# Kernel optimization log

Measured on AMD Instinct MI355X. Metric: run time of the kernel, lower is better.

The kernel has to match this reference:

```python
import jax, jax.numpy as jnp
import numpy as np

EPS = 1e-8

def setup_inputs() -> dict:
    key = jax.random.key(0)
    k1, k2, k3, k4, k5 = jax.random.split(key, 5)
    B, C_in, C_out, H, W, S, K = 16, 128, 128, 128, 128, 512, 3
    return {
        "x": jax.random.normal(k1, (B, C_in, H, W), dtype=jnp.float32),
        "style": jax.random.normal(k2, (B, S), dtype=jnp.float32),
        "weight": jax.random.normal(k3, (1, C_out, C_in, K, K), dtype=jnp.float32),
        "mod_w": jax.random.normal(k4, (C_in, S), dtype=jnp.float32) * 0.05,
        "mod_b": jax.random.normal(k5, (C_in,), dtype=jnp.float32) * 0.05,
    }

def _modulated_weights(style, weight, mod_w, mod_b):
    # style: [B, S] -> s: [B, C_in]
    s = style @ mod_w.T + mod_b
    # w: [B, C_out, C_in, K, K]
    w = weight * s[:, None, :, None, None]
    # demodulation: rsqrt of sum of squares over (C_in, K, K)
    decoef = jax.lax.rsqrt(jnp.sum(w * w, axis=(2, 3, 4)) + EPS)  # [B, C_out]
    return w * decoef[:, :, None, None, None]

def _conv_one(xi, wi):
    # xi: [C_in, H, W], wi: [C_out, C_in, K, K]; 'SAME' padding (K//2)
    out = jax.lax.conv_general_dilated(
        xi[None], wi,
        window_strides=(1, 1), padding="SAME",
        dimension_numbers=("NCHW", "OIHW", "NCHW"))
    return out[0]

def reference(x, style, weight, mod_w, mod_b):
    w = _modulated_weights(style, weight, mod_w, mod_b)  # [B, C_out, C_in, K, K]
    # per-sample conv (equivalent to groups=B grouped conv in torch)
    return jax.vmap(_conv_one)(x, w)  # [B, C_out, H, W]
```

## Files before the change

kernel.cpp:

```cpp
#include <hip/hip_runtime.h>
#include <hip/hip_bf16.h>


#define Bn 16
#define Cc 128
#define HW 128
#define Sv 512

typedef __bf16 bf16x8 __attribute__((ext_vector_type(8)));
typedef float f32x4 __attribute__((ext_vector_type(4)));
typedef unsigned short ushort8 __attribute__((ext_vector_type(8)));

static __device__ __forceinline__ unsigned short bf16bits(float f) {
    return __builtin_bit_cast(unsigned short, __float2bfloat16(f));
}

static __device__ __forceinline__ void gl_lds16(const void* g, void* l) {
    __builtin_amdgcn_global_load_lds(
        (const __attribute__((address_space(1))) unsigned int*)g,
        (__attribute__((address_space(3))) unsigned int*)l, 16, 0, 0);
}

__global__ __launch_bounds__(64) void k_style(const float* __restrict__ style,
                                              const float* __restrict__ mod_w,
                                              const float* __restrict__ mod_b,
                                              float* __restrict__ s_out) {
    int b = blockIdx.x >> 7, ci = blockIdx.x & 127;
    int lane = threadIdx.x;
    const float* st = style + (size_t)b * Sv;
    const float* mw = mod_w + (size_t)ci * Sv;
    float acc = 0.f;
#pragma unroll
    for (int k = 0; k < Sv; k += 64)
        acc += st[k + lane] * mw[k + lane];
#pragma unroll
    for (int off = 32; off > 0; off >>= 1)
        acc += __shfl_down(acc, off, 64);
    if (lane == 0) s_out[b * Cc + ci] = acc + mod_b[ci];
}

__global__ __launch_bounds__(128) void k_mod(const float* __restrict__ weight,
                                             const float* __restrict__ s,
                                             __hip_bfloat16* __restrict__ wsW) {
    int b = blockIdx.x >> 7;
    int co = blockIdx.x & 127;
    int ci = threadIdx.x;
    float sv = s[b * Cc + ci];
    const float* wp = weight + ((size_t)co * Cc + ci) * 9;
    float wv[9];
    float ss = 0.f;
#pragma unroll
    for (int j = 0; j < 9; j++) {
        wv[j] = wp[j] * sv;
        ss += wv[j] * wv[j];
    }
    __shared__ float red[128];
    red[ci] = ss;
    __syncthreads();
    for (int s2 = 64; s2 > 0; s2 >>= 1) {
        if (ci < s2) red[ci] += red[ci + s2];
        __syncthreads();
    }
    float dec = rsqrtf(red[0] + 1e-8f);
    int pos = ((((ci >> 3) ^ (co & 7)) << 3) | (ci & 7));
#pragma unroll
    for (int j = 0; j < 9; j++) {
        wsW[(((size_t)b * 9 + j) * Cc + co) * Cc + pos] = __float2bfloat16(wv[j] * dec);
    }
}

__global__ __launch_bounds__(256, 2) void k_conv(const float* __restrict__ x,
                                                 const __hip_bfloat16* __restrict__ wsW,
                                                 float* __restrict__ out) {
    __shared__ __align__(16) __bf16 Xs[130 * 128];
    __shared__ __align__(16) __bf16 Ws[128 * 128];

    int bx = blockIdx.x;
    int b = bx >> 7, h = bx & 127;
    int t = threadIdx.x;
    int lane = t & 63;
    int wvid = t >> 6;
    int wave_m = wvid >> 1, wave_n = wvid & 1;
    int l15 = lane & 15, quad = lane >> 4;

    f32x4 acc[4][4] = {};

    const float* xb = x + (size_t)b * (Cc * HW * HW);
    const __hip_bfloat16* wbase = wsW + (size_t)b * 9 * (Cc * Cc);

    if (t < 32) {
        int row = (t < 16) ? 0 : 129;
        int g = t & 15;
        *(bf16x8*)(&Xs[row * 128 + g * 8]) = (bf16x8){};
    }

    for (int kh = 0; kh < 3; kh++) {
        int hp = h + kh - 1;
        if ((unsigned)hp >= (unsigned)HW) continue;

        __syncthreads();
        const float* xr = xb + (size_t)hp * HW;
#pragma unroll
        for (int it = 0; it < 8; it++) {
            int id = it * 256 + t;
            int w = id & 127;
            int cig = id >> 7;
            const float* p = xr + (size_t)cig * 8 * (HW * HW) + w;
            ushort8 pk;
#pragma unroll
            for (int j = 0; j < 8; j++)
                pk[j] = bf16bits(p[(size_t)j * (HW * HW)]);
            int row = w + 1;
            int g2 = cig ^ (row & 7);
            *(bf16x8*)(&Xs[row * 128 + (g2 << 3)]) = __builtin_bit_cast(bf16x8, pk);
        }

        for (int kw = 0; kw < 3; kw++) {
            __syncthreads();
            const __hip_bfloat16* wsrc = wbase + (size_t)(kh * 3 + kw) * (Cc * Cc);
#pragma unroll
            for (int it = 0; it < 8; it++) {
                int chunk = wvid * 8 + it;
                gl_lds16(wsrc + chunk * 512 + lane * 8, &Ws[chunk * 512]);
            }
            __syncthreads();
#pragma unroll
            for (int ks = 0; ks < 4; ks++) {
                int kg = ks * 4 + quad;
                bf16x8 a[4], bfr[4];
#pragma unroll
                for (int mi = 0; mi < 4; mi++) {
                    int co = wave_m * 64 + mi * 16 + l15;
                    a[mi] = *(const bf16x8*)(&Ws[co * 128 + ((kg ^ (co & 7)) << 3)]);
                }
#pragma unroll
                for (int ni = 0; ni < 4; ni++) {
                    int row = wave_n * 64 + ni * 16 + l15 + kw;
                    bfr[ni] = *(const bf16x8*)(&Xs[row * 128 + ((kg ^ (row & 7)) << 3)]);
                }
#pragma unroll
                for (int mi = 0; mi < 4; mi++)
#pragma unroll
                    for (int ni = 0; ni < 4; ni++)
                        acc[mi][ni] = __builtin_amdgcn_mfma_f32_16x16x32_bf16(a[mi], bfr[ni], acc[mi][ni], 0, 0, 0);
            }
        }
    }

    float* ob = out + (size_t)b * (Cc * HW * HW) + h * HW;
#pragma unroll
    for (int mi = 0; mi < 4; mi++) {
#pragma unroll
        for (int ni = 0; ni < 4; ni++) {
            int w = wave_n * 64 + ni * 16 + l15;
#pragma unroll
            for (int r = 0; r < 4; r++) {
                int co = wave_m * 64 + mi * 16 + quad * 4 + r;
                ob[(size_t)co * (HW * HW) + w] = acc[mi][ni][r];
            }
        }
    }
}

extern "C" void kernel_launch(void* const* d_in, const int* in_sizes, int n_in,
                              void* d_out, int out_size, void* d_ws, size_t ws_size,
                              hipStream_t stream) {
    const float* x      = (const float*)d_in[0];
    const float* style  = (const float*)d_in[1];
    const float* weight = (const float*)d_in[2];
    const float* mod_w  = (const float*)d_in[3];
    const float* mod_b  = (const float*)d_in[4];
    float* out = (float*)d_out;

    float* s_ws = (float*)d_ws;
    __hip_bfloat16* wsW = (__hip_bfloat16*)((char*)d_ws + 8192);

    k_style<<<Bn * Cc, 64, 0, stream>>>(style, mod_w, mod_b, s_ws);
    k_mod<<<Bn * Cc, 128, 0, stream>>>(weight, s_ws, wsW);
    k_conv<<<Bn * HW, 256, 0, stream>>>(x, wsW, out);
}
```

Before: 299.5 us.

## Compute two output rows per block, sharing weights and four preloaded input rows

Each conv block now covers two output rows with 512 threads. It preloads four bf16 input rows into LDS once and shares each staged 3x3 weight slice across both rows. Horizontal padding moves from extra LDS rows to clamped indices with zeroing, and block indices are remapped so neighbouring blocks share a batch. This halves weight traffic per output row and drops the per-kh input reload and barriers. In exchange LDS grows to about 160KB, which likely allows only one block per CU, and all input loads happen up front with no overlap.

```diff
diff --git a/kernel.cpp b/kernel.cpp
--- a/kernel.cpp
+++ b/kernel.cpp
@@ -69,18 +69,23 @@
     }
 }
 
-__global__ __launch_bounds__(256, 2) void k_conv(const float* __restrict__ x,
+__global__ __launch_bounds__(512, 2) void k_conv(const float* __restrict__ x,
                                                  const __hip_bfloat16* __restrict__ wsW,
                                                  float* __restrict__ out) {
-    __shared__ __align__(16) __bf16 Xs[130 * 128];
+    __shared__ __align__(16) __bf16 Xs[4 * 128 * 128];
     __shared__ __align__(16) __bf16 Ws[128 * 128];
 
-    int bx = blockIdx.x;
-    int b = bx >> 7, h = bx & 127;
+    int bx0 = blockIdx.x;
+    int bx = (bx0 & 7) * 128 + (bx0 >> 3);
+    int b = bx >> 6;
+    int h0 = (bx & 63) << 1;
+
     int t = threadIdx.x;
     int lane = t & 63;
-    int wvid = t >> 6;
-    int wave_m = wvid >> 1, wave_n = wvid & 1;
+    int wv = t >> 6;
+    int m2 = wv >> 2;
+    int th = (wv >> 1) & 1;
+    int n2 = wv & 1;
     int l15 = lane & 15, quad = lane >> 4;
 
     f32x4 acc[4][4] = {};
@@ -88,74 +93,76 @@
     const float* xb = x + (size_t)b * (Cc * HW * HW);
     const __hip_bfloat16* wbase = wsW + (size_t)b * 9 * (Cc * Cc);
 
-    if (t < 32) {
-        int row = (t < 16) ? 0 : 129;
-        int g = t & 15;
-        *(bf16x8*)(&Xs[row * 128 + g * 8]) = (bf16x8){};
+    for (int j = 0; j < 4; j++) {
+        int hp = h0 - 1 + j;
+        bool ok = (unsigned)hp < (unsigned)HW;
+        const float* xr = xb + (size_t)hp * HW;
+#pragma unroll
+        for (int c = 0; c < 4; c++) {
+            int id = c * 512 + t;
+            int w = id & 127;
+            int g = id >> 7;
+            ushort8 pk = {};
+            if (ok) {
+                const float* p = xr + (size_t)g * 8 * (HW * HW) + w;
+#pragma unroll
+                for (int e = 0; e < 8; e++)
+                    pk[e] = bf16bits(p[(size_t)e * (HW * HW)]);
+            }
+            *(bf16x8*)(&Xs[j * 16384 + w * 128 + ((g ^ (w & 7)) << 3)]) =
+                __builtin_bit_cast(bf16x8, pk);
+        }
     }
 
     for (int kh = 0; kh < 3; kh++) {
-        int hp = h + kh - 1;
-        if ((unsigned)hp >= (unsigned)HW) continue;
-
-        __syncthreads();
-        const float* xr = xb + (size_t)hp * HW;
-#pragma unroll
-        for (int it = 0; it < 8; it++) {
-            int id = it * 256 + t;
-            int w = id & 127;
-            int cig = id >> 7;
-            const float* p = xr + (size_t)cig * 8 * (HW * HW) + w;
-            ushort8 pk;
-#pragma unroll
-            for (int j = 0; j < 8; j++)
-                pk[j] = bf16bits(p[(size_t)j * (HW * HW)]);
-            int row = w + 1;
-            int g2 = cig ^ (row & 7);
-            *(bf16x8*)(&Xs[row * 128 + (g2 << 3)]) = __builtin_bit_cast(bf16x8, pk);
-        }
-
+        int xbuf = (kh + th) * 16384;
         for (int kw = 0; kw < 3; kw++) {
             __syncthreads();
             const __hip_bfloat16* wsrc = wbase + (size_t)(kh * 3 + kw) * (Cc * Cc);
 #pragma unroll
-            for (int it = 0; it < 8; it++) {
-                int chunk = wvid * 8 + it;
+            for (int c = 0; c < 4; c++) {
+                int chunk = wv * 4 + c;
                 gl_lds16(wsrc + chunk * 512 + lane * 8, &Ws[chunk * 512]);
             }
             __syncthreads();
 #pragma unroll
             for (int ks = 0; ks < 4; ks++) {
                 int kg = ks * 4 + quad;
-                bf16x8 a[4], bfr[4];
+                bf16x8 a[4], bb[4];
 #pragma unroll
                 for (int mi = 0; mi < 4; mi++) {
-                    int co = wave_m * 64 + mi * 16 + l15;
+                    int co = m2 * 64 + mi * 16 + l15;
                     a[mi] = *(const bf16x8*)(&Ws[co * 128 + ((kg ^ (co & 7)) << 3)]);
                 }
 #pragma unroll
                 for (int ni = 0; ni < 4; ni++) {
-                    int row = wave_n * 64 + ni * 16 + l15 + kw;
-                    bfr[ni] = *(const bf16x8*)(&Xs[row * 128 + ((kg ^ (row & 7)) << 3)]);
+                    int xr = n2 * 64 + ni * 16 + l15 + kw - 1;
+                    int xrc = min(127, max(0, xr));
+                    bf16x8 v = *(const bf16x8*)(
+                        &Xs[xbuf + xrc * 128 + ((kg ^ (xrc & 7)) << 3)]);
+                    if (xr != xrc) v = (bf16x8){};
+                    bb[ni] = v;
                 }
 #pragma unroll
                 for (int mi = 0; mi < 4; mi++)
 #pragma unroll
                     for (int ni = 0; ni < 4; ni++)
-                        acc[mi][ni] = __builtin_amdgcn_mfma_f32_16x16x32_bf16(a[mi], bfr[ni], acc[mi][ni], 0, 0, 0);
+                        acc[mi][ni] = __builtin_amdgcn_mfma_f32_16x16x32_bf16(
+                            a[mi], bb[ni], acc[mi][ni], 0, 0, 0);
             }
         }
     }
 
-    float* ob = out + (size_t)b * (Cc * HW * HW) + h * HW;
+    int h = h0 + th;
+    float* ob = out + (size_t)b * (Cc * HW * HW) + (size_t)h * HW;
 #pragma unroll
     for (int mi = 0; mi < 4; mi++) {
 #pragma unroll
         for (int ni = 0; ni < 4; ni++) {
-            int w = wave_n * 64 + ni * 16 + l15;
+            int w = n2 * 64 + ni * 16 + l15;
 #pragma unroll
             for (int r = 0; r < 4; r++) {
-                int co = wave_m * 64 + mi * 16 + quad * 4 + r;
+                int co = m2 * 64 + mi * 16 + quad * 4 + r;
                 ob[(size_t)co * (HW * HW) + w] = acc[mi][ni][r];
             }
         }
@@ -177,5 +184,5 @@
 
     k_style<<<Bn * Cc, 64, 0, stream>>>(style, mod_w, mod_b, s_ws);
     k_mod<<<Bn * Cc, 128, 0, stream>>>(weight, s_ws, wsW);
-    k_conv<<<Bn * HW, 256, 0, stream>>>(x, wsW, out);
+    k_conv<<<Bn * (HW / 2), 512, 0, stream>>>(x, wsW, out);
 }
```

After: 313.4 us. 4.7% more time.

## Pre-pack weights into MFMA fragment order and load A operands from global

Applied to the files above, without the earlier changes.

The modulation kernel now writes the demodulated bf16 weights in a per-wave MFMA fragment layout, staged through shared memory so the global stores are coalesced. The conv kernel drops the shared-memory weight tile and its per-kw barriers and loads A fragments straight from global/L2 as contiguous 16-byte vectors. With the smaller LDS footprint, occupancy is raised to 4 blocks per CU, and block indices are remapped so neighbouring blocks spread across samples. The risk is added global/L2 latency on the A loads, which the MFMA loop now has to hide, plus possible cache pressure from the changed block order.

```diff
diff --git a/kernel.cpp b/kernel.cpp
--- a/kernel.cpp
+++ b/kernel.cpp
@@ -13,12 +13,6 @@
 
 static __device__ __forceinline__ unsigned short bf16bits(float f) {
     return __builtin_bit_cast(unsigned short, __float2bfloat16(f));
-}
-
-static __device__ __forceinline__ void gl_lds16(const void* g, void* l) {
-    __builtin_amdgcn_global_load_lds(
-        (const __attribute__((address_space(1))) unsigned int*)g,
-        (__attribute__((address_space(3))) unsigned int*)l, 16, 0, 0);
 }
 
 __global__ __launch_bounds__(64) void k_style(const float* __restrict__ style,
@@ -55,6 +49,7 @@
         ss += wv[j] * wv[j];
     }
     __shared__ float red[128];
+    __shared__ __align__(16) __bf16 wo[9 * 128];
     red[ci] = ss;
     __syncthreads();
     for (int s2 = 64; s2 > 0; s2 >>= 1) {
@@ -62,20 +57,31 @@
         __syncthreads();
     }
     float dec = rsqrtf(red[0] + 1e-8f);
-    int pos = ((((ci >> 3) ^ (co & 7)) << 3) | (ci & 7));
 #pragma unroll
-    for (int j = 0; j < 9; j++) {
-        wsW[(((size_t)b * 9 + j) * Cc + co) * Cc + pos] = __float2bfloat16(wv[j] * dec);
+    for (int j = 0; j < 9; j++)
+        wo[j * 128 + ci] = __float2bfloat16(wv[j] * dec);
+    __syncthreads();
+    int fragbase = ((co >> 6) << 4) | (((co >> 4) & 3) << 2);
+#pragma unroll
+    for (int it = 0; it < 2; it++) {
+        int c = it * 128 + ci;
+        if (c < 144) {
+            int j = c >> 4, g = c & 15;
+            bf16x8 chunk = *(const bf16x8*)(&wo[j * 128 + g * 8]);
+            size_t off = (((size_t)b * 9 + j) * 32 + fragbase + (g >> 2)) * 512 +
+                         (size_t)(((g & 3) << 4) | (co & 15)) * 8;
+            *(bf16x8*)(wsW + off) = chunk;
+        }
     }
 }
 
-__global__ __launch_bounds__(256, 2) void k_conv(const float* __restrict__ x,
+__global__ __launch_bounds__(256, 4) void k_conv(const float* __restrict__ x,
                                                  const __hip_bfloat16* __restrict__ wsW,
                                                  float* __restrict__ out) {
     __shared__ __align__(16) __bf16 Xs[130 * 128];
-    __shared__ __align__(16) __bf16 Ws[128 * 128];
 
-    int bx = blockIdx.x;
+    int bx0 = blockIdx.x;
+    int bx = (bx0 & 7) * 256 + (bx0 >> 3);
     int b = bx >> 7, h = bx & 127;
     int t = threadIdx.x;
     int lane = t & 63;
@@ -86,7 +92,8 @@
     f32x4 acc[4][4] = {};
 
     const float* xb = x + (size_t)b * (Cc * HW * HW);
-    const __hip_bfloat16* wbase = wsW + (size_t)b * 9 * (Cc * Cc);
+    const __hip_bfloat16* wb2 =
+        wsW + ((size_t)b * 9) * (32 * 512) + (size_t)(wave_m * 16) * 512 + lane * 8;
 
     if (t < 32) {
         int row = (t < 16) ? 0 : 129;
@@ -114,25 +121,17 @@
             int g2 = cig ^ (row & 7);
             *(bf16x8*)(&Xs[row * 128 + (g2 << 3)]) = __builtin_bit_cast(bf16x8, pk);
         }
+        __syncthreads();
 
         for (int kw = 0; kw < 3; kw++) {
-            __syncthreads();
-            const __hip_bfloat16* wsrc = wbase + (size_t)(kh * 3 + kw) * (Cc * Cc);
-#pragma unroll
-            for (int it = 0; it < 8; it++) {
-                int chunk = wvid * 8 + it;
-                gl_lds16(wsrc + chunk * 512 + lane * 8, &Ws[chunk * 512]);
-            }
-            __syncthreads();
+            const __hip_bfloat16* af = wb2 + (size_t)(kh * 3 + kw) * (32 * 512);
 #pragma unroll
             for (int ks = 0; ks < 4; ks++) {
                 int kg = ks * 4 + quad;
                 bf16x8 a[4], bfr[4];
 #pragma unroll
-                for (int mi = 0; mi < 4; mi++) {
-                    int co = wave_m * 64 + mi * 16 + l15;
-                    a[mi] = *(const bf16x8*)(&Ws[co * 128 + ((kg ^ (co & 7)) << 3)]);
-                }
+                for (int mi = 0; mi < 4; mi++)
+                    a[mi] = *(const bf16x8*)(af + (size_t)(mi * 4 + ks) * 512);
 #pragma unroll
                 for (int ni = 0; ni < 4; ni++) {
                     int row = wave_n * 64 + ni * 16 + l15 + kw;
@@ -142,7 +141,8 @@
                 for (int mi = 0; mi < 4; mi++)
 #pragma unroll
                     for (int ni = 0; ni < 4; ni++)
-                        acc[mi][ni] = __builtin_amdgcn_mfma_f32_16x16x32_bf16(a[mi], bfr[ni], acc[mi][ni], 0, 0, 0);
+                        acc[mi][ni] = __builtin_amdgcn_mfma_f32_16x16x32_bf16(
+                            a[mi], bfr[ni], acc[mi][ni], 0, 0, 0);
             }
         }
     }
```

Result: slower. 375.8 us (+25.5%).
